# Optimization experiments

Measured on AMD Instinct MI355X. Metric: run time of the kernel, lower is better.

## Reference

```python
import jax, jax.numpy as jnp
import numpy as np

B, T, F, L = 8, 2048, 64, 48  # batch, time, numFilters, attentionLen


def setup_inputs() -> dict:
    key = jax.random.key(0)
    k1, k2 = jax.random.split(key)
    he = jax.random.normal(k1, (B, T, F), dtype=jnp.float32)
    # DecoderBlock modeled as a Dense(numFilters) producing the per-step query
    W = jax.random.normal(k2, (F, F), dtype=jnp.float32) / jnp.sqrt(jnp.float32(F))
    b = jnp.zeros((F,), dtype=jnp.float32)
    return {"he": he, "W": W, "b": b}


def reference(he, W, b):
    # he: [B, T, F]. Query at step i: q_i = he[:, i] @ W + b.
    # Window for step i>=1: he[:, max(i-L, 0):i, :]; step 0 attends to he[:, 0, :].
    Bb, Tt, Ff = he.shape
    q = jnp.einsum('btf,fg->btg', he, W) + b            # [B, T, F]

    i = jnp.arange(Tt)[:, None]                          # [T, 1]
    k = jnp.arange(L)[None, :]                           # [1, L]
    rel = i - L + k                                      # window position j = i-L+k (so j in [i-L, i-1])
    valid = jnp.where(i == 0, k == L - 1, rel >= 0)      # step 0: only position 0 (last slot)
    idx = jnp.clip(rel, 0, Tt - 1)                       # [T, L]

    he_win = he[:, idx, :]                               # [B, T, L, F] gathered sliding windows
    scores = jnp.einsum('btlf,btf->btl', he_win, q)      # [B, T, L]
    scores = jnp.where(valid[None], scores, jnp.float32(-1e30))
    w = jax.nn.softmax(scores, axis=-1)                  # softmax over the window (axis=1 in original)
    ctx = jnp.einsum('btl,btlf->btf', w, he_win)         # [B, T, F]
    return ctx
```

## Files before the change

kernel.cpp:

```cpp
#include <hip/hip_runtime.h>
#include <hip/hip_bf16.h>

#define BB 8
#define TT 2048
#define FF 64
#define LL 48
#define TB 64
#define RE 112
#define NW 8
#define NT (NW * 64)

typedef __attribute__((ext_vector_type(8))) short bf16x8;
typedef __attribute__((ext_vector_type(4))) float f32x4;

#define HE_HI 0
#define HE_LO 14336
#define WT_HI 28672
#define WT_LO 36864
#define QQ_HI 45056
#define QQ_LO 53248
#define HET   28672
#define PT    45056
#define RED   61440
#define SMEM_BYTES 62464

__device__ __forceinline__ unsigned short f2b(float x) {
    unsigned int u = __builtin_bit_cast(unsigned int, x);
    return (unsigned short)((u + 0x7FFFu + ((u >> 16) & 1u)) >> 16);
}
__device__ __forceinline__ float b2f(unsigned short h) {
    return __builtin_bit_cast(float, (unsigned int)h << 16);
}

__global__ __launch_bounds__(NT, 1)
void ContextBlock_kernel(const float* __restrict__ he,
                         const float* __restrict__ Wm,
                         const float* __restrict__ bias,
                         float* __restrict__ out)
{
    __shared__ __align__(16) unsigned char smem[SMEM_BYTES];

    const int tid  = threadIdx.x;
    const int wave = tid >> 6;
    const int lane = tid & 63;
    const int bb   = blockIdx.y;
    const int t0   = blockIdx.x * TB;

    const float* heb = he + (size_t)bb * TT * FF;

    const float4* he4 = (const float4*)heb;
    for (int e = tid; e < RE * 16; e += NT) {
        int r = e >> 4, c4 = e & 15;
        int g = t0 - LL + r; g = g < 0 ? 0 : g;
        float4 v = he4[g * 16 + c4];
        unsigned short h0 = f2b(v.x), h1 = f2b(v.y), h2 = f2b(v.z), h3 = f2b(v.w);
        unsigned short l0 = f2b(v.x - b2f(h0)), l1 = f2b(v.y - b2f(h1));
        unsigned short l2 = f2b(v.z - b2f(h2)), l3 = f2b(v.w - b2f(h3));
        unsigned long long pkh = (unsigned long long)h0 | ((unsigned long long)h1 << 16)
                               | ((unsigned long long)h2 << 32) | ((unsigned long long)h3 << 48);
        unsigned long long pkl = (unsigned long long)l0 | ((unsigned long long)l1 << 16)
                               | ((unsigned long long)l2 << 32) | ((unsigned long long)l3 << 48);
        int off = r * 128 + ((((c4 >> 1) ^ (r & 7)) << 4)) + ((c4 & 1) << 3);
        *(unsigned long long*)(smem + HE_HI + off) = pkh;
        *(unsigned long long*)(smem + HE_LO + off) = pkl;
    }
    const float4* w4 = (const float4*)Wm;
    for (int e = tid; e < 1024; e += NT) {
        int f = e >> 4, g4 = e & 15;
        float4 v = w4[e];
        float vv[4] = {v.x, v.y, v.z, v.w};
        #pragma unroll
        for (int i = 0; i < 4; ++i) {
            int g = g4 * 4 + i;
            unsigned short hi = f2b(vv[i]);
            unsigned short lo = f2b(vv[i] - b2f(hi));
            int off = g * 128 + ((((f >> 3) ^ (g & 7)) << 4)) + ((f & 7) << 1);
            *(unsigned short*)(smem + WT_HI + off) = hi;
            *(unsigned short*)(smem + WT_LO + off) = lo;
        }
    }
    __syncthreads();

    const int l15 = lane & 15;
    const int lhi = lane >> 4;

    #pragma unroll
    for (int s = 0; s < 2; ++s) {
        int q = wave * 2 + s;
        int mt = q >> 2, nt = q & 3;
        f32x4 acc = (f32x4){0.f, 0.f, 0.f, 0.f};
        int arow = LL + mt * 16 + l15;
        int colg = nt * 16 + l15;
        #pragma unroll
        for (int kf = 0; kf < 2; ++kf) {
            int chunk = 4 * kf + lhi;
            int offA = arow * 128 + ((chunk ^ (arow & 7)) << 4);
            int offB = colg * 128 + ((chunk ^ (colg & 7)) << 4);
            bf16x8 ah = *(const bf16x8*)(smem + HE_HI + offA);
            bf16x8 al = *(const bf16x8*)(smem + HE_LO + offA);
            bf16x8 bh = *(const bf16x8*)(smem + WT_HI + offB);
            bf16x8 bl = *(const bf16x8*)(smem + WT_LO + offB);
            acc = __builtin_amdgcn_mfma_f32_16x16x32_bf16(ah, bh, acc, 0, 0, 0);
            acc = __builtin_amdgcn_mfma_f32_16x16x32_bf16(ah, bl, acc, 0, 0, 0);
            acc = __builtin_amdgcn_mfma_f32_16x16x32_bf16(al, bh, acc, 0, 0, 0);
        }
        float bv = bias[colg];
        #pragma unroll
        for (int i = 0; i < 4; ++i) {
            int tok = mt * 16 + lhi * 4 + i;
            float qv = acc[i] + bv;
            unsigned short hi = f2b(qv);
            unsigned short lo = f2b(qv - b2f(hi));
            int off = tok * 128 + ((((colg >> 3) ^ (tok & 7)) << 4)) + ((colg & 7) << 1);
            *(unsigned short*)(smem + QQ_HI + off) = hi;
            *(unsigned short*)(smem + QQ_LO + off) = lo;
        }
    }
    __syncthreads();

    const int ct = wave >> 1, pp = wave & 1;
    const int tok = ct * 16 + l15;
    f32x4 sc[2];
    #pragma unroll
    for (int u = 0; u < 2; ++u) {
        int rt = ct + 2 * pp + u;
        f32x4 acc = (f32x4){0.f, 0.f, 0.f, 0.f};
        int arow = rt * 16 + l15;
        #pragma unroll
        for (int kf = 0; kf < 2; ++kf) {
            int chunk = 4 * kf + lhi;
            int offA = arow * 128 + ((chunk ^ (arow & 7)) << 4);
            int offB = tok * 128 + ((chunk ^ (tok & 7)) << 4);
            bf16x8 ah = *(const bf16x8*)(smem + HE_HI + offA);
            bf16x8 al = *(const bf16x8*)(smem + HE_LO + offA);
            bf16x8 bh = *(const bf16x8*)(smem + QQ_HI + offB);
            bf16x8 bl = *(const bf16x8*)(smem + QQ_LO + offB);
            acc = __builtin_amdgcn_mfma_f32_16x16x32_bf16(ah, bh, acc, 0, 0, 0);
            acc = __builtin_amdgcn_mfma_f32_16x16x32_bf16(ah, bl, acc, 0, 0, 0);
            acc = __builtin_amdgcn_mfma_f32_16x16x32_bf16(al, bh, acc, 0, 0, 0);
        }
        sc[u] = acc;
    }
    float m = -1e30f;
    #pragma unroll
    for (int u = 0; u < 2; ++u) {
        int rt = ct + 2 * pp + u;
        #pragma unroll
        for (int i = 0; i < 4; ++i) {
            int r_ext = rt * 16 + lhi * 4 + i;
            int l = r_ext - tok;
            bool valid = (t0 == 0 && tok == 0) ? (r_ext == LL - 1)
                                               : (l >= 0 && l < LL && (t0 + r_ext) >= LL);
            float s = valid ? sc[u][i] : -1e30f;
            sc[u][i] = s;
            m = fmaxf(m, s);
        }
    }
    m = fmaxf(m, __shfl_xor(m, 16));
    m = fmaxf(m, __shfl_xor(m, 32));
    float sum = 0.f;
    #pragma unroll
    for (int u = 0; u < 2; ++u)
        #pragma unroll
        for (int i = 0; i < 4; ++i)
            sum += __expf(sc[u][i] - m);
    sum += __shfl_xor(sum, 16);
    sum += __shfl_xor(sum, 32);
    if (lane < 16) {
        float2 ms = make_float2(m, sum);
        *(float2*)(smem + RED + tok * 16 + pp * 8) = ms;
    }
    __syncthreads();

    {
        float2 p0 = *(const float2*)(smem + RED + tok * 16 + 0);
        float2 p1 = *(const float2*)(smem + RED + tok * 16 + 8);
        float M = fmaxf(p0.x, p1.x);
        float T = p0.y * __expf(p0.x - M) + p1.y * __expf(p1.x - M);
        float invT = 1.0f / T;
        #pragma unroll
        for (int u = 0; u < 2; ++u) {
            int rt = ct + 2 * pp + u;
            int rbase = rt * 16 + lhi * 4;
            unsigned short w0 = f2b(__expf(sc[u][0] - M) * invT);
            unsigned short w1 = f2b(__expf(sc[u][1] - M) * invT);
            unsigned short w2 = f2b(__expf(sc[u][2] - M) * invT);
            unsigned short w3 = f2b(__expf(sc[u][3] - M) * invT);
            unsigned long long pk = (unsigned long long)w0 | ((unsigned long long)w1 << 16)
                                  | ((unsigned long long)w2 << 32) | ((unsigned long long)w3 << 48);
            *(unsigned long long*)(smem + PT + tok * 256
                + ((((rbase >> 3) ^ (tok & 7)) << 4)) + ((rbase & 7) << 1)) = pk;
            int zbase = (((rt + 4) & 7) * 16) + lhi * 4;
            *(unsigned long long*)(smem + PT + tok * 256
                + ((((zbase >> 3) ^ (tok & 7)) << 4)) + ((zbase & 7) << 1)) = 0ull;
        }
    }
    for (int e = tid; e < RE * 64; e += NT) {
        int r = e >> 6, f = e & 63;
        unsigned short h = *(const unsigned short*)
            (smem + HE_HI + r * 128 + ((((f >> 3) ^ (r & 7)) << 4)) + ((f & 7) << 1));
        *(unsigned short*)
            (smem + HET + f * 256 + ((((r >> 3) ^ (f & 7)) << 4)) + ((r & 7) << 1)) = h;
    }
    if (tid < 128) {
        int f = tid >> 1, c = 14 + (tid & 1);
        *(f32x4*)(smem + HET + f * 256 + ((c ^ (f & 7)) << 4)) = (f32x4){0.f, 0.f, 0.f, 0.f};
    }
    __syncthreads();

    #pragma unroll
    for (int s2 = 0; s2 < 2; ++s2) {
        int t = wave * 2 + s2;
        int mt = t >> 2, nt = t & 3;
        f32x4 acc = (f32x4){0.f, 0.f, 0.f, 0.f};
        int arow = mt * 16 + l15;
        int brow = nt * 16 + l15;
        int kf0 = mt >> 1;
        int nkf = (mt & 1) ? 3 : 2;
        for (int kk = 0; kk < nkf; ++kk) {
            int chunk = 4 * (kf0 + kk) + lhi;
            bf16x8 a  = *(const bf16x8*)(smem + PT  + arow * 256 + ((chunk ^ (arow & 7)) << 4));
            bf16x8 bo = *(const bf16x8*)(smem + HET + brow * 256 + ((chunk ^ (brow & 7)) << 4));
            acc = __builtin_amdgcn_mfma_f32_16x16x32_bf16(a, bo, acc, 0, 0, 0);
        }
        #pragma unroll
        for (int i = 0; i < 4; ++i) {
            int tk = mt * 16 + lhi * 4 + i;
            out[((size_t)bb * TT + t0 + tk) * FF + nt * 16 + l15] = acc[i];
        }
    }
}

extern "C" void kernel_launch(void* const* d_in, const int* in_sizes, int n_in,
                              void* d_out, int out_size, void* d_ws, size_t ws_size,
                              hipStream_t stream) {
    const float* he   = (const float*)d_in[0];
    const float* Wm   = (const float*)d_in[1];
    const float* bias = (const float*)d_in[2];
    float* out        = (float*)d_out;

    dim3 grid(TT / TB, BB);
    ContextBlock_kernel<<<grid, NT, 0, stream>>>(he, Wm, bias, out);
}
```

Measured before the change: 11.97 us.

## Halve token tile per block and remap waves for two blocks per CU

```diff
diff --git a/kernel.cpp b/kernel.cpp
--- a/kernel.cpp
+++ b/kernel.cpp
@@ -5,8 +5,8 @@
 #define TT 2048
 #define FF 64
 #define LL 48
-#define TB 64
-#define RE 112
+#define TB 32
+#define RE (TB + LL)
 #define NW 8
 #define NT (NW * 64)
 
@@ -14,15 +14,15 @@
 typedef __attribute__((ext_vector_type(4))) float f32x4;
 
 #define HE_HI 0
-#define HE_LO 14336
-#define WT_HI 28672
-#define WT_LO 36864
-#define QQ_HI 45056
-#define QQ_LO 53248
-#define HET   28672
-#define PT    45056
-#define RED   61440
-#define SMEM_BYTES 62464
+#define HE_LO 10240
+#define WT_HI 20480
+#define WT_LO 28672
+#define QQ_HI 36864
+#define QQ_LO 40960
+#define HET   20480
+#define PT    36864
+#define RED   45056
+#define SMEM_BYTES 46080
 
 __device__ __forceinline__ unsigned short f2b(float x) {
     unsigned int u = __builtin_bit_cast(unsigned int, x);
@@ -32,7 +32,7 @@
     return __builtin_bit_cast(float, (unsigned int)h << 16);
 }
 
-__global__ __launch_bounds__(NT, 1)
+__global__ __launch_bounds__(NT, 2)
 void ContextBlock_kernel(const float* __restrict__ he,
                          const float* __restrict__ Wm,
                          const float* __restrict__ bias,
@@ -84,10 +84,8 @@
     const int l15 = lane & 15;
     const int lhi = lane >> 4;
 
-    #pragma unroll
-    for (int s = 0; s < 2; ++s) {
-        int q = wave * 2 + s;
-        int mt = q >> 2, nt = q & 3;
+    {
+        int mt = wave >> 2, nt = wave & 3;
         f32x4 acc = (f32x4){0.f, 0.f, 0.f, 0.f};
         int arow = LL + mt * 16 + l15;
         int colg = nt * 16 + l15;
@@ -118,12 +116,11 @@
     }
     __syncthreads();
 
-    const int ct = wave >> 1, pp = wave & 1;
+    const int ct = wave >> 2, uu = wave & 3;
+    const int rt = ct + uu;
     const int tok = ct * 16 + l15;
-    f32x4 sc[2];
-    #pragma unroll
-    for (int u = 0; u < 2; ++u) {
-        int rt = ct + 2 * pp + u;
+    f32x4 sc;
+    {
         f32x4 acc = (f32x4){0.f, 0.f, 0.f, 0.f};
         int arow = rt * 16 + l15;
         #pragma unroll
@@ -139,61 +136,56 @@
             acc = __builtin_amdgcn_mfma_f32_16x16x32_bf16(ah, bl, acc, 0, 0, 0);
             acc = __builtin_amdgcn_mfma_f32_16x16x32_bf16(al, bh, acc, 0, 0, 0);
         }
-        sc[u] = acc;
+        sc = acc;
     }
     float m = -1e30f;
     #pragma unroll
-    for (int u = 0; u < 2; ++u) {
-        int rt = ct + 2 * pp + u;
-        #pragma unroll
-        for (int i = 0; i < 4; ++i) {
-            int r_ext = rt * 16 + lhi * 4 + i;
-            int l = r_ext - tok;
-            bool valid = (t0 == 0 && tok == 0) ? (r_ext == LL - 1)
-                                               : (l >= 0 && l < LL && (t0 + r_ext) >= LL);
-            float s = valid ? sc[u][i] : -1e30f;
-            sc[u][i] = s;
-            m = fmaxf(m, s);
-        }
+    for (int i = 0; i < 4; ++i) {
+        int r_ext = rt * 16 + lhi * 4 + i;
+        int l = r_ext - tok;
+        bool valid = (t0 == 0 && tok == 0) ? (r_ext == LL - 1)
+                                           : (l >= 0 && l < LL && (t0 + r_ext) >= LL);
+        float s = valid ? sc[i] : -1e30f;
+        sc[i] = s;
+        m = fmaxf(m, s);
     }
     m = fmaxf(m, __shfl_xor(m, 16));
     m = fmaxf(m, __shfl_xor(m, 32));
     float sum = 0.f;
     #pragma unroll
-    for (int u = 0; u < 2; ++u)
-        #pragma unroll
-        for (int i = 0; i < 4; ++i)
-            sum += __expf(sc[u][i] - m);
+    for (int i = 0; i < 4; ++i)
+        sum += __expf(sc[i] - m);
     sum += __shfl_xor(sum, 16);
     sum += __shfl_xor(sum, 32);
-    if (lane < 16) {
-        float2 ms = make_float2(m, sum);
-        *(float2*)(smem + RED + tok * 16 + pp * 8) = ms;
-    }
-    __syncthreads();
-
-    {
-        float2 p0 = *(const float2*)(smem + RED + tok * 16 + 0);
-        float2 p1 = *(const float2*)(smem + RED + tok * 16 + 8);
-        float M = fmaxf(p0.x, p1.x);
-        float T = p0.y * __expf(p0.x - M) + p1.y * __expf(p1.x - M);
+    if (lane < 16)
+        *(float2*)(smem + RED + tok * 32 + uu * 8) = make_float2(m, sum);
+    __syncthreads();
+
+    {
+        float M = -1e30f;
+        float2 p[4];
+        #pragma unroll
+        for (int u = 0; u < 4; ++u) {
+            p[u] = *(const float2*)(smem + RED + tok * 32 + u * 8);
+            M = fmaxf(M, p[u].x);
+        }
+        float T = 0.f;
+        #pragma unroll
+        for (int u = 0; u < 4; ++u)
+            T += p[u].y * __expf(p[u].x - M);
         float invT = 1.0f / T;
-        #pragma unroll
-        for (int u = 0; u < 2; ++u) {
-            int rt = ct + 2 * pp + u;
-            int rbase = rt * 16 + lhi * 4;
-            unsigned short w0 = f2b(__expf(sc[u][0] - M) * invT);
-            unsigned short w1 = f2b(__expf(sc[u][1] - M) * invT);
-            unsigned short w2 = f2b(__expf(sc[u][2] - M) * invT);
-            unsigned short w3 = f2b(__expf(sc[u][3] - M) * invT);
-            unsigned long long pk = (unsigned long long)w0 | ((unsigned long long)w1 << 16)
-                                  | ((unsigned long long)w2 << 32) | ((unsigned long long)w3 << 48);
-            *(unsigned long long*)(smem + PT + tok * 256
-                + ((((rbase >> 3) ^ (tok & 7)) << 4)) + ((rbase & 7) << 1)) = pk;
-            int zbase = (((rt + 4) & 7) * 16) + lhi * 4;
-            *(unsigned long long*)(smem + PT + tok * 256
-                + ((((zbase >> 3) ^ (tok & 7)) << 4)) + ((zbase & 7) << 1)) = 0ull;
-        }
+        int rbase = rt * 16 + lhi * 4;
+        unsigned short w0 = f2b(__expf(sc[0] - M) * invT);
+        unsigned short w1 = f2b(__expf(sc[1] - M) * invT);
+        unsigned short w2 = f2b(__expf(sc[2] - M) * invT);
+        unsigned short w3 = f2b(__expf(sc[3] - M) * invT);
+        unsigned long long pk = (unsigned long long)w0 | ((unsigned long long)w1 << 16)
+                              | ((unsigned long long)w2 << 32) | ((unsigned long long)w3 << 48);
+        *(unsigned long long*)(smem + PT + tok * 256
+            + ((((rbase >> 3) ^ (tok & 7)) << 4)) + ((rbase & 7) << 1)) = pk;
+        int zbase = (((rt + 4) & 7) * 16) + lhi * 4;
+        *(unsigned long long*)(smem + PT + tok * 256
+            + ((((zbase >> 3) ^ (tok & 7)) << 4)) + ((zbase & 7) << 1)) = 0ull;
     }
     for (int e = tid; e < RE * 64; e += NT) {
         int r = e >> 6, f = e & 63;
@@ -202,23 +194,16 @@
         *(unsigned short*)
             (smem + HET + f * 256 + ((((r >> 3) ^ (f & 7)) << 4)) + ((r & 7) << 1)) = h;
     }
-    if (tid < 128) {
-        int f = tid >> 1, c = 14 + (tid & 1);
-        *(f32x4*)(smem + HET + f * 256 + ((c ^ (f & 7)) << 4)) = (f32x4){0.f, 0.f, 0.f, 0.f};
-    }
-    __syncthreads();
-
-    #pragma unroll
-    for (int s2 = 0; s2 < 2; ++s2) {
-        int t = wave * 2 + s2;
-        int mt = t >> 2, nt = t & 3;
+    __syncthreads();
+
+    {
+        int mt = wave >> 2, nt = wave & 3;
         f32x4 acc = (f32x4){0.f, 0.f, 0.f, 0.f};
         int arow = mt * 16 + l15;
         int brow = nt * 16 + l15;
-        int kf0 = mt >> 1;
-        int nkf = (mt & 1) ? 3 : 2;
-        for (int kk = 0; kk < nkf; ++kk) {
-            int chunk = 4 * (kf0 + kk) + lhi;
+        #pragma unroll
+        for (int kk = 0; kk < 2; ++kk) {
+            int chunk = 2 * mt + 4 * kk + lhi;
             bf16x8 a  = *(const bf16x8*)(smem + PT  + arow * 256 + ((chunk ^ (arow & 7)) << 4));
             bf16x8 bo = *(const bf16x8*)(smem + HET + brow * 256 + ((chunk ^ (brow & 7)) << 4));
             acc = __builtin_amdgcn_mfma_f32_16x16x32_bf16(a, bo, acc, 0, 0, 0);
```

Measured after the change: 12.32 us. 2.9% more time.
